# Optimization experiments

Measured on AMD Instinct MI355X. Metric: run time of the kernel, lower is better.

The kernel has to match this reference:

```python
import jax, jax.numpy as jnp
import numpy as np

N_NODES = 50000
N_EDGES = 800000
IN_DIM = 256
HID = 64
NEG_SLOPE = 0.2


def setup_inputs() -> dict:
    key = jax.random.key(0)
    ks = jax.random.split(key, 16)
    s = lambda d: 1.0 / np.sqrt(d)
    x = jax.random.normal(ks[0], (N_NODES, IN_DIM), dtype=jnp.float32)
    src = jax.random.randint(ks[1], (N_EDGES,), 0, N_NODES, dtype=jnp.int32)
    dst = jax.random.randint(ks[2], (N_EDGES,), 0, N_NODES, dtype=jnp.int32)
    # layer 0: in 256 -> 4 heads x 64, no residual, ELU
    W0 = jax.random.normal(ks[3], (IN_DIM, 4 * HID), dtype=jnp.float32) * s(IN_DIM)
    al0 = jax.random.normal(ks[4], (4, HID), dtype=jnp.float32) * s(HID)
    ar0 = jax.random.normal(ks[5], (4, HID), dtype=jnp.float32) * s(HID)
    b0 = jnp.zeros((4 * HID,), dtype=jnp.float32)
    # layer 1: in 256 -> 4 heads x 64, identity residual (256 == 4*64), ELU
    W1 = jax.random.normal(ks[6], (4 * HID, 4 * HID), dtype=jnp.float32) * s(4 * HID)
    al1 = jax.random.normal(ks[7], (4, HID), dtype=jnp.float32) * s(HID)
    ar1 = jax.random.normal(ks[8], (4, HID), dtype=jnp.float32) * s(HID)
    b1 = jnp.zeros((4 * HID,), dtype=jnp.float32)
    # layer 2 (output): in 256 -> 1 head x 64, linear residual, no activation
    W2 = jax.random.normal(ks[9], (4 * HID, HID), dtype=jnp.float32) * s(4 * HID)
    al2 = jax.random.normal(ks[10], (1, HID), dtype=jnp.float32) * s(HID)
    ar2 = jax.random.normal(ks[11], (1, HID), dtype=jnp.float32) * s(HID)
    b2 = jnp.zeros((HID,), dtype=jnp.float32)
    res_w2 = jax.random.normal(ks[12], (4 * HID, HID), dtype=jnp.float32) * s(4 * HID)
    return {"x": x, "src": src, "dst": dst,
            "W0": W0, "al0": al0, "ar0": ar0, "b0": b0,
            "W1": W1, "al1": al1, "ar1": ar1, "b1": b1,
            "W2": W2, "al2": al2, "ar2": ar2, "b2": b2,
            "res_w2": res_w2}


def gat_layer(h, src, dst, W, al, ar, bias, residual, res_w, activation):
    H, D = al.shape
    feat = (h @ W).reshape(-1, H, D)               # [N,H,D]
    el = jnp.sum(feat * al[None], axis=-1)         # [N,H]
    er = jnp.sum(feat * ar[None], axis=-1)         # [N,H]
    e = jax.nn.leaky_relu(el[src] + er[dst], NEG_SLOPE)  # [E,H]
    # segment softmax over incoming edges of each destination node
    emax = jax.ops.segment_max(e, dst, num_segments=N_NODES)  # [N,H]
    ee = jnp.exp(e - emax[dst])
    denom = jax.ops.segment_sum(ee, dst, num_segments=N_NODES)
    alpha = ee / denom[dst]                        # [E,H]
    msg = feat[src] * alpha[..., None]             # [E,H,D]
    out = jax.ops.segment_sum(msg, dst, num_segments=N_NODES)  # [N,H,D]
    if residual:
        if res_w is not None:
            out = out + (h @ res_w).reshape(-1, 1, D)
        else:
            out = out + h.reshape(-1, H, D)
    out = out + bias.reshape(H, D)
    if activation:
        out = jax.nn.elu(out)
    return out.reshape(-1, H * D)                  # flatten(1)


def reference(x, src, dst, W0, al0, ar0, b0, W1, al1, ar1, b1,
              W2, al2, ar2, b2, res_w2):
    h = gat_layer(x, src, dst, W0, al0, ar0, b0, False, None, True)
    h = gat_layer(h, src, dst, W1, al1, ar1, b1, True, None, True)
    h = gat_layer(h, src, dst, W2, al2, ar2, b2, True, res_w2, False)
    return h  # [N, 64]
```

## Files before the change

### kernel.cpp

```cpp
#include <hip/hip_runtime.h>
#include <math.h>

#define NNODES 50000
#define NEDGES 800000
#define NSB 49
#define NPACK 640
#define NCVT 3125
#define EBH 3125
#define NBM 391
#define SCB 1563
#define AGGB 2048

__device__ __forceinline__ float leaky(float x) { return x > 0.f ? x : 0.2f * x; }

__device__ __forceinline__ ushort f2bf(float f) {
    unsigned u = __float_as_uint(f);
    return (ushort)((u + 0x7fffu + ((u >> 16) & 1u)) >> 16);
}
__device__ __forceinline__ float bf2f(ushort u) {
    return __uint_as_float((unsigned)u << 16);
}

typedef const __attribute__((address_space(1))) void* gptr_t;
typedef __attribute__((address_space(3))) void* lptr_t;

__global__ __launch_bounds__(256) void front_kernel(
    const int* __restrict__ dst, int* __restrict__ counts,
    const float* __restrict__ W0, const float* __restrict__ W1, const float* __restrict__ W2,
    const float* __restrict__ Wr, ushort* __restrict__ Bt0, ushort* __restrict__ Bt1,
    ushort* __restrict__ Bt2, const float* __restrict__ x, ushort* __restrict__ xb) {
    using ushort8v = __attribute__((ext_vector_type(8))) unsigned short;
    int t = threadIdx.x;
    if (blockIdx.x < EBH) {
        int e = blockIdx.x * 256 + t;
        if (e < NEDGES) atomicAdd(&counts[dst[e]], 1);
    } else if (blockIdx.x < EBH + NPACK) {
        int idx = (blockIdx.x - EBH) * 256 + t;
        if (idx < 65536) {
            int n = idx >> 8, k = idx & 255;
            Bt0[idx] = f2bf(W0[k * 256 + n]);
        } else if (idx < 131072) {
            int j = idx - 65536;
            int n = j >> 8, k = j & 255;
            Bt1[j] = f2bf(W1[k * 256 + n]);
        } else {
            int j = idx - 131072;
            int n = j >> 8, k = j & 255;
            Bt2[j] = f2bf(n < 64 ? W2[k * 64 + n] : Wr[k * 64 + (n - 64)]);
        }
    } else {
        size_t j = (size_t)(blockIdx.x - EBH - NPACK) * 4096 + t * 16;
        float4 a0 = *reinterpret_cast<const float4*>(x + j);
        float4 a1 = *reinterpret_cast<const float4*>(x + j + 4);
        float4 a2 = *reinterpret_cast<const float4*>(x + j + 8);
        float4 a3 = *reinterpret_cast<const float4*>(x + j + 12);
        union { ushort8v v; ushort u[8]; } p0, p1;
        p0.u[0] = f2bf(a0.x); p0.u[1] = f2bf(a0.y); p0.u[2] = f2bf(a0.z); p0.u[3] = f2bf(a0.w);
        p0.u[4] = f2bf(a1.x); p0.u[5] = f2bf(a1.y); p0.u[6] = f2bf(a1.z); p0.u[7] = f2bf(a1.w);
        p1.u[0] = f2bf(a2.x); p1.u[1] = f2bf(a2.y); p1.u[2] = f2bf(a2.z); p1.u[3] = f2bf(a2.w);
        p1.u[4] = f2bf(a3.x); p1.u[5] = f2bf(a3.y); p1.u[6] = f2bf(a3.z); p1.u[7] = f2bf(a3.w);
        *reinterpret_cast<ushort8v*>(xb + j) = p0.v;
        *reinterpret_cast<ushort8v*>(xb + j + 8) = p1.v;
    }
}

__global__ __launch_bounds__(256) void scan_partial(const int* __restrict__ counts,
                                                    int* __restrict__ bsum, int Nn) {
    int b = blockIdx.x, t = threadIdx.x;
    int base = b * 1024;
    int v = 0;
#pragma unroll
    for (int i = 0; i < 4; ++i) {
        int idx = base + t + 256 * i;
        if (idx < Nn) v += counts[idx];
    }
    for (int o = 32; o; o >>= 1) v += __shfl_xor(v, o);
    __shared__ int ws[4];
    if ((t & 63) == 0) ws[t >> 6] = v;
    __syncthreads();
    if (t == 0) bsum[b] = ws[0] + ws[1] + ws[2] + ws[3];
}

__global__ __launch_bounds__(256) void scan_final(const int* __restrict__ counts,
                                                  const int* __restrict__ bsum,
                                                  int* __restrict__ row_start, int Nn, int nB) {
    __shared__ int off_s;
    __shared__ int tsum[256];
    int b = blockIdx.x, t = threadIdx.x;
    if (t == 0) {
        int o = 0;
        for (int i = 0; i < b; ++i) o += bsum[i];
        off_s = o;
    }
    int base = b * 1024 + t * 4;
    int c0 = 0, c1 = 0, c2 = 0, c3 = 0;
    if (base + 3 < Nn) {
        int4 c = *reinterpret_cast<const int4*>(counts + base);
        c0 = c.x; c1 = c.y; c2 = c.z; c3 = c.w;
    } else {
        if (base + 0 < Nn) c0 = counts[base + 0];
        if (base + 1 < Nn) c1 = counts[base + 1];
        if (base + 2 < Nn) c2 = counts[base + 2];
        if (base + 3 < Nn) c3 = counts[base + 3];
    }
    int s0 = c0, s1 = s0 + c1, s2 = s1 + c2, s3 = s2 + c3;
    tsum[t] = s3;
    __syncthreads();
    for (int o = 1; o < 256; o <<= 1) {
        int u = (t >= o) ? tsum[t - o] : 0;
        __syncthreads();
        tsum[t] += u;
        __syncthreads();
    }
    int o = off_s + tsum[t] - s3;
    if (base + 3 < Nn) {
        *reinterpret_cast<int4*>(row_start + base) = make_int4(o, o + s0, o + s1, o + s2);
    } else {
        if (base + 0 < Nn) row_start[base + 0] = o;
        if (base + 1 < Nn) row_start[base + 1] = o + s0;
        if (base + 2 < Nn) row_start[base + 2] = o + s1;
        if (base + 3 < Nn) row_start[base + 3] = o + s2;
    }
    if (b == nB - 1 && t == 255) row_start[Nn] = off_s + tsum[255];
}

template <bool SCAT>
__global__ __launch_bounds__(512) void gemm_wide(const ushort* __restrict__ Ab,
                                                 const ushort* __restrict__ Bt,
                                                 const float* __restrict__ al,
                                                 const float* __restrict__ ar,
                                                 ushort* __restrict__ featb,
                                                 float* __restrict__ el, float* __restrict__ er,
                                                 int Nrows,
                                                 const int* __restrict__ srcv,
                                                 const int* __restrict__ dstv,
                                                 const int* __restrict__ row_start,
                                                 int* __restrict__ cursor,
                                                 ushort* __restrict__ csr_src) {
    using bf16x8 = __attribute__((ext_vector_type(8))) short;
    using f32x4 = __attribute__((ext_vector_type(4))) float;
    __shared__ ushort As[8192];
    __shared__ ushort Bs[16384];
    if constexpr (SCAT) {
        if (blockIdx.x >= NBM) {
            int e = (blockIdx.x - NBM) * 512 + threadIdx.x;
            if (e < NEDGES) {
                int d = dstv[e];
                int pos = row_start[d] + atomicAdd(&cursor[d], 1);
                csr_src[pos] = (ushort)srcv[e];
            }
            return;
        }
    }
    const int tid = threadIdx.x;
    const int lane = tid & 63;
    const int wave = tid >> 6;
    const int wr = wave >> 2, wc = wave & 3;
    const int q = lane >> 4, li = lane & 15;
    const int r0 = blockIdx.x * 128;

    f32x4 acc[4][4];
#pragma unroll
    for (int i = 0; i < 4; ++i)
#pragma unroll
        for (int j = 0; j < 4; ++j) acc[i][j] = (f32x4){0.f, 0.f, 0.f, 0.f};

    for (int kk = 0; kk < 256; kk += 64) {
        __syncthreads();
#pragma unroll
        for (int j = 0; j < 2; ++j) {
            int c = wave * 128 + j * 64 + lane;
            int mr = c & 15, kg = (c >> 4) & 7, mf = c >> 7;
            const ushort* gp = Ab + (size_t)(r0 + mf * 16 + mr) * 256 + kk + kg * 8;
            void* lp = (char*)As + (size_t)(wave * 2 + j) * 1024;
            __builtin_amdgcn_global_load_lds((gptr_t)gp, (lptr_t)lp, 16, 0, 0);
        }
#pragma unroll
        for (int j = 0; j < 4; ++j) {
            int c = wave * 256 + j * 64 + lane;
            int nr = c & 15, kg = (c >> 4) & 7, nf = c >> 7;
            const ushort* gp = Bt + (size_t)(nf * 16 + nr) * 256 + kk + kg * 8;
            void* lp = (char*)Bs + (size_t)(wave * 4 + j) * 1024;
            __builtin_amdgcn_global_load_lds((gptr_t)gp, (lptr_t)lp, 16, 0, 0);
        }
        __syncthreads();
#pragma unroll
        for (int t = 0; t < 2; ++t) {
            const int kc = t * 4 + q;
            bf16x8 af[4], bfv[4];
#pragma unroll
            for (int f = 0; f < 4; ++f) {
                af[f] = *reinterpret_cast<const bf16x8*>(
                    &As[(((wr * 4 + f) * 8 + kc) * 16 + li) * 8]);
                bfv[f] = *reinterpret_cast<const bf16x8*>(
                    &Bs[(((wc * 4 + f) * 8 + kc) * 16 + li) * 8]);
            }
#pragma unroll
            for (int f = 0; f < 4; ++f)
#pragma unroll
                for (int f2 = 0; f2 < 4; ++f2)
                    acc[f][f2] =
                        __builtin_amdgcn_mfma_f32_16x16x32_bf16(af[f], bfv[f2], acc[f][f2], 0, 0, 0);
        }
    }

    float alv[4], arv[4];
#pragma unroll
    for (int f2 = 0; f2 < 4; ++f2) {
        alv[f2] = al[wc * 64 + f2 * 16 + li];
        arv[f2] = ar[wc * 64 + f2 * 16 + li];
    }
#pragma unroll
    for (int f = 0; f < 4; ++f) {
#pragma unroll
        for (int r = 0; r < 4; ++r) {
            int row = r0 + wr * 64 + f * 16 + q * 4 + r;
            bool ok = row < Nrows;
            float elp = 0.f, erp = 0.f;
#pragma unroll
            for (int f2 = 0; f2 < 4; ++f2) {
                float v = acc[f][f2][r];
                elp = fmaf(v, alv[f2], elp);
                erp = fmaf(v, arv[f2], erp);
                if (ok) featb[(size_t)row * 256 + (f2 * 16 + li) * 4 + wc] = f2bf(v);
            }
#pragma unroll
            for (int o = 1; o < 16; o <<= 1) {
                elp += __shfl_xor(elp, o);
                erp += __shfl_xor(erp, o);
            }
            if (ok && li == 0) {
                el[row * 4 + wc] = elp;
                er[row * 4 + wc] = erp;
            }
        }
    }
}

__global__ __launch_bounds__(256) void gemm_l2(const ushort* __restrict__ Ab,
                                               const ushort* __restrict__ Bt,
                                               const float* __restrict__ al,
                                               const float* __restrict__ ar,
                                               ushort* __restrict__ featb,
                                               float* __restrict__ el, float* __restrict__ er,
                                               float* __restrict__ resid, int Nrows) {
    using bf16x8 = __attribute__((ext_vector_type(8))) short;
    using f32x4 = __attribute__((ext_vector_type(4))) float;
    __shared__ ushort As[8192];
    __shared__ ushort Bs[8192];
    const int tid = threadIdx.x;
    const int lane = tid & 63;
    const int wave = tid >> 6;
    const int wr = wave >> 1, wc = wave & 1;
    const int q = lane >> 4, li = lane & 15;
    const int r0 = blockIdx.x * 128;

    f32x4 acc[4][4];
#pragma unroll
    for (int i = 0; i < 4; ++i)
#pragma unroll
        for (int j = 0; j < 4; ++j) acc[i][j] = (f32x4){0.f, 0.f, 0.f, 0.f};

    for (int kk = 0; kk < 256; kk += 64) {
        __syncthreads();
#pragma unroll
        for (int j = 0; j < 4; ++j) {
            int c = (wave * 4 + j) * 64 + lane;
            int mr = c & 15, kg = (c >> 4) & 7, mf = c >> 7;
            const ushort* gp = Ab + (size_t)(r0 + mf * 16 + mr) * 256 + kk + kg * 8;
            void* lp = (char*)As + (size_t)(wave * 4 + j) * 1024;
            __builtin_amdgcn_global_load_lds((gptr_t)gp, (lptr_t)lp, 16, 0, 0);
        }
#pragma unroll
        for (int j = 0; j < 4; ++j) {
            int c = (wave * 4 + j) * 64 + lane;
            int nr = c & 15, kg = (c >> 4) & 7, nf = c >> 7;
            const ushort* gp = Bt + (size_t)(nf * 16 + nr) * 256 + kk + kg * 8;
            void* lp = (char*)Bs + (size_t)(wave * 4 + j) * 1024;
            __builtin_amdgcn_global_load_lds((gptr_t)gp, (lptr_t)lp, 16, 0, 0);
        }
        __syncthreads();
#pragma unroll
        for (int t = 0; t < 2; ++t) {
            const int kc = t * 4 + q;
            bf16x8 af[4], bfv[4];
#pragma unroll
            for (int f = 0; f < 4; ++f) {
                af[f] = *reinterpret_cast<const bf16x8*>(
                    &As[(((wr * 4 + f) * 8 + kc) * 16 + li) * 8]);
                bfv[f] = *reinterpret_cast<const bf16x8*>(
                    &Bs[(((wc * 4 + f) * 8 + kc) * 16 + li) * 8]);
            }
#pragma unroll
            for (int f = 0; f < 4; ++f)
#pragma unroll
                for (int f2 = 0; f2 < 4; ++f2)
                    acc[f][f2] =
                        __builtin_amdgcn_mfma_f32_16x16x32_bf16(af[f], bfv[f2], acc[f][f2], 0, 0, 0);
        }
    }

    if (wc == 0) {
        float alv[4], arv[4];
#pragma unroll
        for (int f2 = 0; f2 < 4; ++f2) {
            alv[f2] = al[f2 * 16 + li];
            arv[f2] = ar[f2 * 16 + li];
        }
#pragma unroll
        for (int f = 0; f < 4; ++f) {
#pragma unroll
            for (int r = 0; r < 4; ++r) {
                int row = r0 + wr * 64 + f * 16 + q * 4 + r;
                bool ok = row < Nrows;
                float elp = 0.f, erp = 0.f;
#pragma unroll
                for (int f2 = 0; f2 < 4; ++f2) {
                    float v = acc[f][f2][r];
                    elp = fmaf(v, alv[f2], elp);
                    erp = fmaf(v, arv[f2], erp);
                    if (ok) featb[(size_t)row * 64 + f2 * 16 + li] = f2bf(v);
                }
#pragma unroll
                for (int o = 1; o < 16; o <<= 1) {
                    elp += __shfl_xor(elp, o);
                    erp += __shfl_xor(erp, o);
                }
                if (ok && li == 0) {
                    el[row] = elp;
                    er[row] = erp;
                }
            }
        }
    } else {
#pragma unroll
        for (int f = 0; f < 4; ++f) {
#pragma unroll
            for (int r = 0; r < 4; ++r) {
                int row = r0 + wr * 64 + f * 16 + q * 4 + r;
                if (row < Nrows) {
#pragma unroll
                    for (int f2 = 0; f2 < 4; ++f2)
                        resid[(size_t)row * 64 + f2 * 16 + li] = acc[f][f2][r];
                }
            }
        }
    }
}

template <int RES, bool ACT>
__global__ __launch_bounds__(256) void agg4_kernel(
    const ushort* __restrict__ featb, const float* __restrict__ el,
    const float* __restrict__ er, const int* __restrict__ row_start,
    const ushort* __restrict__ csr_src, const ushort* __restrict__ resbuf,
    const float* __restrict__ bias, ushort* __restrict__ out, int Nn) {
    using ushort8v = __attribute__((ext_vector_type(8))) unsigned short;
    __shared__ float wbuf[4][256];
    __shared__ int obuf[4][64];
    const int wv = threadIdx.x >> 6, lane = threadIdx.x & 63;
    const int g = lane >> 5, li = lane & 31;

    float2 bv0 = *reinterpret_cast<const float2*>(bias + (g * 2 + 0) * 64 + li * 2);
    float2 bv1 = *reinterpret_cast<const float2*>(bias + (g * 2 + 1) * 64 + li * 2);

    for (int node = blockIdx.x * 4 + wv; node < Nn; node += gridDim.x * 4) {
        int begin = row_start[node], end = row_start[node + 1];
        float4 ern = *(reinterpret_cast<const float4*>(er) + node);

        float denom[4] = {0.f, 0.f, 0.f, 0.f};
        float acc[2][4] = {{0.f, 0.f, 0.f, 0.f}, {0.f, 0.f, 0.f, 0.f}};

        for (int c = begin; c < end; c += 64) {
            int nE = min(64, end - c);
            float4 w = make_float4(0.f, 0.f, 0.f, 0.f);
            int s = 0;
            if (lane < nE) {
                s = csr_src[c + lane];
                float4 e4 = *(reinterpret_cast<const float4*>(el) + s);
                w.x = __expf(leaky(e4.x + ern.x));
                w.y = __expf(leaky(e4.y + ern.y));
                w.z = __expf(leaky(e4.z + ern.z));
                w.w = __expf(leaky(e4.w + ern.w));
            }
            denom[0] += w.x; denom[1] += w.y; denom[2] += w.z; denom[3] += w.w;
            obuf[wv][lane] = s * 256;
            *reinterpret_cast<float4*>(&wbuf[wv][lane * 4]) = w;
            __asm__ volatile("s_waitcnt lgkmcnt(0)" ::: "memory");

#pragma unroll 8
            for (int e2 = 0; e2 < nE; e2 += 2) {
                int e = e2 + g;
                float4 we = make_float4(0.f, 0.f, 0.f, 0.f);
                int off = 0;
                if (e < nE) {
                    off = obuf[wv][e];
                    we = *reinterpret_cast<const float4*>(&wbuf[wv][e * 4]);
                }
                ushort8v v = *reinterpret_cast<const ushort8v*>(featb + off + li * 8);
                acc[0][0] = fmaf(we.x, bf2f(v[0]), acc[0][0]);
                acc[0][1] = fmaf(we.y, bf2f(v[1]), acc[0][1]);
                acc[0][2] = fmaf(we.z, bf2f(v[2]), acc[0][2]);
                acc[0][3] = fmaf(we.w, bf2f(v[3]), acc[0][3]);
                acc[1][0] = fmaf(we.x, bf2f(v[4]), acc[1][0]);
                acc[1][1] = fmaf(we.y, bf2f(v[5]), acc[1][1]);
                acc[1][2] = fmaf(we.z, bf2f(v[6]), acc[1][2]);
                acc[1][3] = fmaf(we.w, bf2f(v[7]), acc[1][3]);
            }
            __asm__ volatile("" ::: "memory");
        }

#pragma unroll
        for (int j = 0; j < 2; ++j)
#pragma unroll
            for (int h = 0; h < 4; ++h) acc[j][h] += __shfl_xor(acc[j][h], 32);
#pragma unroll
        for (int h = 0; h < 4; ++h)
            for (int o = 32; o; o >>= 1) denom[h] += __shfl_xor(denom[h], o);

        bool has = end > begin;
#pragma unroll
        for (int hh = 0; hh < 2; ++hh) {
            int h = g * 2 + hh;
            float d0 = denom[h];
            float o0 = has ? acc[0][h] / d0 : 0.f;
            float o1 = has ? acc[1][h] / d0 : 0.f;
            int dbase = h * 64 + li * 2;
            if constexpr (RES == 1) {
                unsigned rv = *reinterpret_cast<const unsigned*>(resbuf + (size_t)node * 256 + dbase);
                o0 += bf2f((ushort)(rv & 0xffffu));
                o1 += bf2f((ushort)(rv >> 16));
            }
            float2 bvv = hh == 0 ? bv0 : bv1;
            o0 += bvv.x; o1 += bvv.y;
            if constexpr (ACT) {
                o0 = o0 > 0.f ? o0 : __expf(o0) - 1.f;
                o1 = o1 > 0.f ? o1 : __expf(o1) - 1.f;
            }
            unsigned pk = (unsigned)f2bf(o0) | ((unsigned)f2bf(o1) << 16);
            *reinterpret_cast<unsigned*>(out + (size_t)node * 256 + dbase) = pk;
        }
    }
}

__global__ __launch_bounds__(256) void agg1_kernel(
    const ushort* __restrict__ featb, const float* __restrict__ el,
    const float* __restrict__ er, const int* __restrict__ row_start,
    const ushort* __restrict__ csr_src, const float* __restrict__ resbuf,
    const float* __restrict__ bias, float* __restrict__ out, int Nn) {
    __shared__ float wbuf[4][64];
    __shared__ int obuf[4][64];
    const int wv = threadIdx.x >> 6, lane = threadIdx.x & 63;
    const int g = lane >> 4, li = lane & 15;

    float4 bv = *reinterpret_cast<const float4*>(bias + li * 4);

    for (int node = blockIdx.x * 4 + wv; node < Nn; node += gridDim.x * 4) {
        int begin = row_start[node], end = row_start[node + 1];
        float ern = er[node];
        float denom = 0.f;
        float acc[4] = {0.f, 0.f, 0.f, 0.f};

        for (int c = begin; c < end; c += 64) {
            int nE = min(64, end - c);
            float w = 0.f;
            int s = 0;
            if (lane < nE) {
                s = csr_src[c + lane];
                w = __expf(leaky(el[s] + ern));
            }
            denom += w;
            obuf[wv][lane] = s * 64;
            wbuf[wv][lane] = w;
            __asm__ volatile("s_waitcnt lgkmcnt(0)" ::: "memory");

#pragma unroll 4
            for (int e4i = 0; e4i < nE; e4i += 4) {
                int e = e4i + g;
                float we = 0.f;
                int off = 0;
                if (e < nE) {
                    off = obuf[wv][e];
                    we = wbuf[wv][e];
                }
                ushort4 v = *reinterpret_cast<const ushort4*>(featb + off + li * 4);
                acc[0] = fmaf(we, bf2f(v.x), acc[0]);
                acc[1] = fmaf(we, bf2f(v.y), acc[1]);
                acc[2] = fmaf(we, bf2f(v.z), acc[2]);
                acc[3] = fmaf(we, bf2f(v.w), acc[3]);
            }
            __asm__ volatile("" ::: "memory");
        }

#pragma unroll
        for (int j = 0; j < 4; ++j) {
            acc[j] += __shfl_xor(acc[j], 16);
            acc[j] += __shfl_xor(acc[j], 32);
        }
        for (int o = 32; o; o >>= 1) denom += __shfl_xor(denom, o);

        if (g == 0) {
            bool has = end > begin;
            float4 rv = *reinterpret_cast<const float4*>(resbuf + (size_t)node * 64 + li * 4);
            float4 o4;
            o4.x = (has ? acc[0] / denom : 0.f) + rv.x + bv.x;
            o4.y = (has ? acc[1] / denom : 0.f) + rv.y + bv.y;
            o4.z = (has ? acc[2] / denom : 0.f) + rv.z + bv.z;
            o4.w = (has ? acc[3] / denom : 0.f) + rv.w + bv.w;
            *reinterpret_cast<float4*>(out + (size_t)node * 64 + li * 4) = o4;
        }
    }
}

extern "C" void kernel_launch(void* const* d_in, const int* in_sizes, int n_in, void* d_out,
                              int out_size, void* d_ws, size_t ws_size, hipStream_t stream) {
    const float* x   = (const float*)d_in[0];
    const int* src   = (const int*)d_in[1];
    const int* dst   = (const int*)d_in[2];
    const float* W0  = (const float*)d_in[3];
    const float* al0 = (const float*)d_in[4];
    const float* ar0 = (const float*)d_in[5];
    const float* b0  = (const float*)d_in[6];
    const float* W1  = (const float*)d_in[7];
    const float* al1 = (const float*)d_in[8];
    const float* ar1 = (const float*)d_in[9];
    const float* b1  = (const float*)d_in[10];
    const float* W2  = (const float*)d_in[11];
    const float* al2 = (const float*)d_in[12];
    const float* ar2 = (const float*)d_in[13];
    const float* b2  = (const float*)d_in[14];
    const float* Wr2 = (const float*)d_in[15];
    float* out = (float*)d_out;

    char* w = (char*)d_ws;
    size_t off = 0;
    auto alloc = [&](size_t bytes) -> char* {
        char* p = w + off;
        off += (bytes + 255) & ~(size_t)255;
        return p;
    };
    ushort* xb      = (ushort*)alloc((size_t)NNODES * 256 * 2);
    ushort* hbuf    = (ushort*)alloc((size_t)NNODES * 256 * 2);
    ushort* featb   = (ushort*)alloc((size_t)NNODES * 256 * 2);
    float* resid    = (float*)alloc((size_t)NNODES * 64 * 4);
    float* el       = (float*)alloc((size_t)NNODES * 4 * 4);
    float* er       = (float*)alloc((size_t)NNODES * 4 * 4);
    ushort* Bt0     = (ushort*)alloc(65536 * 2);
    ushort* Bt1     = (ushort*)alloc(65536 * 2);
    ushort* Bt2     = (ushort*)alloc(32768 * 2);
    int* counts     = (int*)alloc((size_t)NNODES * 4 * 2);
    int* cursor     = counts + NNODES;
    int* row_start  = (int*)alloc((size_t)(NNODES + 1) * 4);
    int* bsum       = (int*)alloc(64 * 4);
    ushort* csr_src = (ushort*)alloc((size_t)NEDGES * 2);

    hipMemsetAsync(counts, 0, (size_t)NNODES * 4 * 2, stream);

    front_kernel<<<EBH + NPACK + NCVT, 256, 0, stream>>>(dst, counts, W0, W1, W2, Wr2,
                                                         Bt0, Bt1, Bt2, x, xb);
    scan_partial<<<NSB, 256, 0, stream>>>(counts, bsum, NNODES);
    scan_final<<<NSB, 256, 0, stream>>>(counts, bsum, row_start, NNODES, NSB);

    gemm_wide<true><<<NBM + SCB, 512, 0, stream>>>(xb, Bt0, al0, ar0, featb, el, er, NNODES,
                                                   src, dst, row_start, cursor, csr_src);
    agg4_kernel<0, true><<<AGGB, 256, 0, stream>>>(featb, el, er, row_start, csr_src,
                                                   nullptr, b0, hbuf, NNODES);
    gemm_wide<false><<<NBM, 512, 0, stream>>>(hbuf, Bt1, al1, ar1, featb, el, er, NNODES,
                                              nullptr, nullptr, nullptr, nullptr, nullptr);
    agg4_kernel<1, true><<<AGGB, 256, 0, stream>>>(featb, el, er, row_start, csr_src,
                                                   hbuf, b1, hbuf, NNODES);
    gemm_l2<<<NBM, 256, 0, stream>>>(hbuf, Bt2, al2, ar2, featb, el, er, resid, NNODES);
    agg1_kernel<<<AGGB, 256, 0, stream>>>(featb, el, er, row_start, csr_src,
                                          resid, b2, out, NNODES);
}
```

Baseline: 425.2 us.

## Map two destination nodes per wavefront in aggregation kernels

The aggregation kernels now give each half-wave (32 lanes) its own destination node instead of a whole wave per node. The grid-stride loop is replaced by a fixed grid of 6250 blocks with eight nodes per block. Each half-wave gathers full 256-wide bf16 rows itself, so the cross-half reduction of accumulators goes away and per-node edge chunks shrink to 32. The two halves share a loop bound equal to the larger degree, so an imbalance between paired nodes leaves lanes idle. The grid also assumes the node count divides evenly, with no bounds check.

```diff
diff --git a/kernel.cpp b/kernel.cpp
--- a/kernel.cpp
+++ b/kernel.cpp
@@ -9,7 +9,7 @@
 #define EBH 3125
 #define NBM 391
 #define SCB 1563
-#define AGGB 2048
+#define NBA 6250
 
 __device__ __forceinline__ float leaky(float x) { return x > 0.f ? x : 0.2f * x; }
 
@@ -355,90 +355,96 @@
     const ushort* __restrict__ csr_src, const ushort* __restrict__ resbuf,
     const float* __restrict__ bias, ushort* __restrict__ out, int Nn) {
     using ushort8v = __attribute__((ext_vector_type(8))) unsigned short;
-    __shared__ float wbuf[4][256];
-    __shared__ int obuf[4][64];
+    __shared__ float4 wbuf[4][2][32];
+    __shared__ int obuf[4][2][32];
     const int wv = threadIdx.x >> 6, lane = threadIdx.x & 63;
     const int g = lane >> 5, li = lane & 31;
-
-    float2 bv0 = *reinterpret_cast<const float2*>(bias + (g * 2 + 0) * 64 + li * 2);
-    float2 bv1 = *reinterpret_cast<const float2*>(bias + (g * 2 + 1) * 64 + li * 2);
-
-    for (int node = blockIdx.x * 4 + wv; node < Nn; node += gridDim.x * 4) {
-        int begin = row_start[node], end = row_start[node + 1];
-        float4 ern = *(reinterpret_cast<const float4*>(er) + node);
-
-        float denom[4] = {0.f, 0.f, 0.f, 0.f};
-        float acc[2][4] = {{0.f, 0.f, 0.f, 0.f}, {0.f, 0.f, 0.f, 0.f}};
-
-        for (int c = begin; c < end; c += 64) {
-            int nE = min(64, end - c);
-            float4 w = make_float4(0.f, 0.f, 0.f, 0.f);
-            int s = 0;
-            if (lane < nE) {
-                s = csr_src[c + lane];
-                float4 e4 = *(reinterpret_cast<const float4*>(el) + s);
-                w.x = __expf(leaky(e4.x + ern.x));
-                w.y = __expf(leaky(e4.y + ern.y));
-                w.z = __expf(leaky(e4.z + ern.z));
-                w.w = __expf(leaky(e4.w + ern.w));
-            }
-            denom[0] += w.x; denom[1] += w.y; denom[2] += w.z; denom[3] += w.w;
-            obuf[wv][lane] = s * 256;
-            *reinterpret_cast<float4*>(&wbuf[wv][lane * 4]) = w;
-            __asm__ volatile("s_waitcnt lgkmcnt(0)" ::: "memory");
-
-#pragma unroll 8
-            for (int e2 = 0; e2 < nE; e2 += 2) {
-                int e = e2 + g;
-                float4 we = make_float4(0.f, 0.f, 0.f, 0.f);
-                int off = 0;
-                if (e < nE) {
-                    off = obuf[wv][e];
-                    we = *reinterpret_cast<const float4*>(&wbuf[wv][e * 4]);
-                }
-                ushort8v v = *reinterpret_cast<const ushort8v*>(featb + off + li * 8);
-                acc[0][0] = fmaf(we.x, bf2f(v[0]), acc[0][0]);
-                acc[0][1] = fmaf(we.y, bf2f(v[1]), acc[0][1]);
-                acc[0][2] = fmaf(we.z, bf2f(v[2]), acc[0][2]);
-                acc[0][3] = fmaf(we.w, bf2f(v[3]), acc[0][3]);
-                acc[1][0] = fmaf(we.x, bf2f(v[4]), acc[1][0]);
-                acc[1][1] = fmaf(we.y, bf2f(v[5]), acc[1][1]);
-                acc[1][2] = fmaf(we.z, bf2f(v[6]), acc[1][2]);
-                acc[1][3] = fmaf(we.w, bf2f(v[7]), acc[1][3]);
-            }
-            __asm__ volatile("" ::: "memory");
-        }
-
-#pragma unroll
-        for (int j = 0; j < 2; ++j)
-#pragma unroll
-            for (int h = 0; h < 4; ++h) acc[j][h] += __shfl_xor(acc[j][h], 32);
-#pragma unroll
-        for (int h = 0; h < 4; ++h)
-            for (int o = 32; o; o >>= 1) denom[h] += __shfl_xor(denom[h], o);
-
-        bool has = end > begin;
-#pragma unroll
-        for (int hh = 0; hh < 2; ++hh) {
-            int h = g * 2 + hh;
-            float d0 = denom[h];
-            float o0 = has ? acc[0][h] / d0 : 0.f;
-            float o1 = has ? acc[1][h] / d0 : 0.f;
-            int dbase = h * 64 + li * 2;
-            if constexpr (RES == 1) {
-                unsigned rv = *reinterpret_cast<const unsigned*>(resbuf + (size_t)node * 256 + dbase);
-                o0 += bf2f((ushort)(rv & 0xffffu));
-                o1 += bf2f((ushort)(rv >> 16));
-            }
-            float2 bvv = hh == 0 ? bv0 : bv1;
-            o0 += bvv.x; o1 += bvv.y;
-            if constexpr (ACT) {
-                o0 = o0 > 0.f ? o0 : __expf(o0) - 1.f;
-                o1 = o1 > 0.f ? o1 : __expf(o1) - 1.f;
-            }
-            unsigned pk = (unsigned)f2bf(o0) | ((unsigned)f2bf(o1) << 16);
-            *reinterpret_cast<unsigned*>(out + (size_t)node * 256 + dbase) = pk;
-        }
+    const int node = blockIdx.x * 8 + wv * 2 + g;
+
+    float2 bvh[4];
+#pragma unroll
+    for (int h = 0; h < 4; ++h)
+        bvh[h] = *reinterpret_cast<const float2*>(bias + h * 64 + li * 2);
+
+    const int begin = row_start[node], end = row_start[node + 1];
+    const float4 ern = *(reinterpret_cast<const float4*>(er) + node);
+
+    float dsum[4] = {0.f, 0.f, 0.f, 0.f};
+    float acc[8] = {0.f, 0.f, 0.f, 0.f, 0.f, 0.f, 0.f, 0.f};
+
+    int c = begin;
+    int rem = end - begin;
+    int remo = __shfl_xor(rem, 32);
+    int nmax = rem > remo ? rem : remo;
+
+    while (nmax > 0) {
+        int nE = rem < 0 ? 0 : (rem < 32 ? rem : 32);
+        int nEmax = nmax < 32 ? nmax : 32;
+        float4 w = make_float4(0.f, 0.f, 0.f, 0.f);
+        int s = 0;
+        if (li < nE) {
+            s = csr_src[c + li];
+            float4 e4 = *(reinterpret_cast<const float4*>(el) + s);
+            w.x = __expf(leaky(e4.x + ern.x));
+            w.y = __expf(leaky(e4.y + ern.y));
+            w.z = __expf(leaky(e4.z + ern.z));
+            w.w = __expf(leaky(e4.w + ern.w));
+        }
+        dsum[0] += w.x; dsum[1] += w.y; dsum[2] += w.z; dsum[3] += w.w;
+        obuf[wv][g][li] = s * 256;
+        wbuf[wv][g][li] = w;
+        __asm__ volatile("s_waitcnt lgkmcnt(0)" ::: "memory");
+
+#pragma unroll 4
+        for (int e = 0; e < nEmax; ++e) {
+            int off = obuf[wv][g][e];
+            float4 we = wbuf[wv][g][e];
+            ushort8v v = *reinterpret_cast<const ushort8v*>(featb + off + li * 8);
+            acc[0] = fmaf(we.x, bf2f(v[0]), acc[0]);
+            acc[1] = fmaf(we.y, bf2f(v[1]), acc[1]);
+            acc[2] = fmaf(we.z, bf2f(v[2]), acc[2]);
+            acc[3] = fmaf(we.w, bf2f(v[3]), acc[3]);
+            acc[4] = fmaf(we.x, bf2f(v[4]), acc[4]);
+            acc[5] = fmaf(we.y, bf2f(v[5]), acc[5]);
+            acc[6] = fmaf(we.z, bf2f(v[6]), acc[6]);
+            acc[7] = fmaf(we.w, bf2f(v[7]), acc[7]);
+        }
+        __asm__ volatile("" ::: "memory");
+        c += 32; rem -= 32; nmax -= 32;
+    }
+
+#pragma unroll
+    for (int h = 0; h < 4; ++h) {
+        dsum[h] += __shfl_xor(dsum[h], 1);
+        dsum[h] += __shfl_xor(dsum[h], 2);
+        dsum[h] += __shfl_xor(dsum[h], 4);
+        dsum[h] += __shfl_xor(dsum[h], 8);
+        dsum[h] += __shfl_xor(dsum[h], 16);
+    }
+
+    const bool has = end > begin;
+    float o8[8];
+#pragma unroll
+    for (int j = 0; j < 8; ++j) o8[j] = has ? acc[j] / dsum[j & 3] : 0.f;
+#pragma unroll
+    for (int h = 0; h < 4; ++h) {
+        if constexpr (RES == 1) {
+            unsigned rv = *reinterpret_cast<const unsigned*>(
+                resbuf + (size_t)node * 256 + h * 64 + li * 2);
+            o8[h]     += bf2f((ushort)(rv & 0xffffu));
+            o8[4 + h] += bf2f((ushort)(rv >> 16));
+        }
+        o8[h]     += bvh[h].x;
+        o8[4 + h] += bvh[h].y;
+    }
+    if constexpr (ACT) {
+#pragma unroll
+        for (int j = 0; j < 8; ++j) o8[j] = o8[j] > 0.f ? o8[j] : __expf(o8[j]) - 1.f;
+    }
+#pragma unroll
+    for (int h = 0; h < 4; ++h) {
+        unsigned pk = (unsigned)f2bf(o8[h]) | ((unsigned)f2bf(o8[4 + h]) << 16);
+        *reinterpret_cast<unsigned*>(out + (size_t)node * 256 + h * 64 + li * 2) = pk;
     }
 }
 
@@ -447,68 +453,63 @@
     const float* __restrict__ er, const int* __restrict__ row_start,
     const ushort* __restrict__ csr_src, const float* __restrict__ resbuf,
     const float* __restrict__ bias, float* __restrict__ out, int Nn) {
-    __shared__ float wbuf[4][64];
-    __shared__ int obuf[4][64];
+    __shared__ float wbuf[4][2][32];
+    __shared__ int obuf[4][2][32];
     const int wv = threadIdx.x >> 6, lane = threadIdx.x & 63;
-    const int g = lane >> 4, li = lane & 15;
-
-    float4 bv = *reinterpret_cast<const float4*>(bias + li * 4);
-
-    for (int node = blockIdx.x * 4 + wv; node < Nn; node += gridDim.x * 4) {
-        int begin = row_start[node], end = row_start[node + 1];
-        float ern = er[node];
-        float denom = 0.f;
-        float acc[4] = {0.f, 0.f, 0.f, 0.f};
-
-        for (int c = begin; c < end; c += 64) {
-            int nE = min(64, end - c);
-            float w = 0.f;
-            int s = 0;
-            if (lane < nE) {
-                s = csr_src[c + lane];
-                w = __expf(leaky(el[s] + ern));
-            }
-            denom += w;
-            obuf[wv][lane] = s * 64;
-            wbuf[wv][lane] = w;
-            __asm__ volatile("s_waitcnt lgkmcnt(0)" ::: "memory");
+    const int g = lane >> 5, li = lane & 31;
+    const int node = blockIdx.x * 8 + wv * 2 + g;
+
+    float2 bv = *reinterpret_cast<const float2*>(bias + li * 2);
+
+    const int begin = row_start[node], end = row_start[node + 1];
+    const float ern = er[node];
+
+    float dsum = 0.f;
+    float acc0 = 0.f, acc1 = 0.f;
+
+    int c = begin;
+    int rem = end - begin;
+    int remo = __shfl_xor(rem, 32);
+    int nmax = rem > remo ? rem : remo;
+
+    while (nmax > 0) {
+        int nE = rem < 0 ? 0 : (rem < 32 ? rem : 32);
+        int nEmax = nmax < 32 ? nmax : 32;
+        float w = 0.f;
+        int s = 0;
+        if (li < nE) {
+            s = csr_src[c + li];
+            w = __expf(leaky(el[s] + ern));
+        }
+        dsum += w;
+        obuf[wv][g][li] = s * 64;
+        wbuf[wv][g][li] = w;
+        __asm__ volatile("s_waitcnt lgkmcnt(0)" ::: "memory");
 
 #pragma unroll 4
-            for (int e4i = 0; e4i < nE; e4i += 4) {
-                int e = e4i + g;
-                float we = 0.f;
-                int off = 0;
-                if (e < nE) {
-                    off = obuf[wv][e];
-                    we = wbuf[wv][e];
-                }
-                ushort4 v = *reinterpret_cast<const ushort4*>(featb + off + li * 4);
-                acc[0] = fmaf(we, bf2f(v.x), acc[0]);
-                acc[1] = fmaf(we, bf2f(v.y), acc[1]);
-                acc[2] = fmaf(we, bf2f(v.z), acc[2]);
-                acc[3] = fmaf(we, bf2f(v.w), acc[3]);
-            }
-            __asm__ volatile("" ::: "memory");
-        }
-
-#pragma unroll
-        for (int j = 0; j < 4; ++j) {
-            acc[j] += __shfl_xor(acc[j], 16);
-            acc[j] += __shfl_xor(acc[j], 32);
-        }
-        for (int o = 32; o; o >>= 1) denom += __shfl_xor(denom, o);
-
-        if (g == 0) {
-            bool has = end > begin;
-            float4 rv = *reinterpret_cast<const float4*>(resbuf + (size_t)node * 64 + li * 4);
-            float4 o4;
-            o4.x = (has ? acc[0] / denom : 0.f) + rv.x + bv.x;
-            o4.y = (has ? acc[1] / denom : 0.f) + rv.y + bv.y;
-            o4.z = (has ? acc[2] / denom : 0.f) + rv.z + bv.z;
-            o4.w = (has ? acc[3] / denom : 0.f) + rv.w + bv.w;
-            *reinterpret_cast<float4*>(out + (size_t)node * 64 + li * 4) = o4;
-        }
-    }
+        for (int e = 0; e < nEmax; ++e) {
+            int off = obuf[wv][g][e];
+            float we = wbuf[wv][g][e];
+            unsigned v = *reinterpret_cast<const unsigned*>(featb + off + li * 2);
+            acc0 = fmaf(we, bf2f((ushort)(v & 0xffffu)), acc0);
+            acc1 = fmaf(we, bf2f((ushort)(v >> 16)), acc1);
+        }
+        __asm__ volatile("" ::: "memory");
+        c += 32; rem -= 32; nmax -= 32;
+    }
+
+    dsum += __shfl_xor(dsum, 1);
+    dsum += __shfl_xor(dsum, 2);
+    dsum += __shfl_xor(dsum, 4);
+    dsum += __shfl_xor(dsum, 8);
+    dsum += __shfl_xor(dsum, 16);
+
+    const bool has = end > begin;
+    float2 rv = *reinterpret_cast<const float2*>(resbuf + (size_t)node * 64 + li * 2);
+    float2 o2;
+    o2.x = (has ? acc0 / dsum : 0.f) + rv.x + bv.x;
+    o2.y = (has ? acc1 / dsum : 0.f) + rv.y + bv.y;
+    *reinterpret_cast<float2*>(out + (size_t)node * 64 + li * 2) = o2;
 }
 
 extern "C" void kernel_launch(void* const* d_in, const int* in_sizes, int n_in, void* d_out,
@@ -562,13 +563,13 @@
 
     gemm_wide<true><<<NBM + SCB, 512, 0, stream>>>(xb, Bt0, al0, ar0, featb, el, er, NNODES,
                                                    src, dst, row_start, cursor, csr_src);
-    agg4_kernel<0, true><<<AGGB, 256, 0, stream>>>(featb, el, er, row_start, csr_src,
-                                                   nullptr, b0, hbuf, NNODES);
+    agg4_kernel<0, true><<<NBA, 256, 0, stream>>>(featb, el, er, row_start, csr_src,
+                                                  nullptr, b0, hbuf, NNODES);
     gemm_wide<false><<<NBM, 512, 0, stream>>>(hbuf, Bt1, al1, ar1, featb, el, er, NNODES,
                                               nullptr, nullptr, nullptr, nullptr, nullptr);
-    agg4_kernel<1, true><<<AGGB, 256, 0, stream>>>(featb, el, er, row_start, csr_src,
-                                                   hbuf, b1, hbuf, NNODES);
+    agg4_kernel<1, true><<<NBA, 256, 0, stream>>>(featb, el, er, row_start, csr_src,
+                                                  hbuf, b1, hbuf, NNODES);
     gemm_l2<<<NBM, 256, 0, stream>>>(hbuf, Bt2, al2, ar2, featb, el, er, resid, NNODES);
-    agg1_kernel<<<AGGB, 256, 0, stream>>>(featb, el, er, row_start, csr_src,
-                                          resid, b2, out, NNODES);
-}
+    agg1_kernel<<<NBA, 256, 0, stream>>>(featb, el, er, row_start, csr_src,
+                                         resid, b2, out, NNODES);
+}
```

Result: faster. 403.7 us (-5.1%).
